# Optimization experiments

Hardware: AMD Instinct MI355X
Metric: run time of the kernel (lower is better)

Reference implementation:

```python
import jax, jax.numpy as jnp
import numpy as np

D_MODEL = 1024
N_HEADS = 16
D_HEAD = 64


def setup_inputs() -> dict:
    key = jax.random.key(0)
    ks = jax.random.split(key, 5)
    B, T = 2, 2048
    scale = 1.0 / np.sqrt(D_MODEL)
    x = jax.random.normal(ks[0], (B, T, D_MODEL), dtype=jnp.float32)
    Wq = jax.random.normal(ks[1], (N_HEADS * D_HEAD, D_MODEL), dtype=jnp.float32) * scale
    Wk = jax.random.normal(ks[2], (N_HEADS * D_HEAD, D_MODEL), dtype=jnp.float32) * scale
    Wv = jax.random.normal(ks[3], (N_HEADS * D_HEAD, D_MODEL), dtype=jnp.float32) * scale
    Wo = jax.random.normal(ks[4], (D_MODEL, N_HEADS * D_HEAD), dtype=jnp.float32) * scale
    return {"x": x, "Wq": Wq, "Wk": Wk, "Wv": Wv, "Wo": Wo}


def reference(x, Wq, Wk, Wv, Wo):
    B, T, D = x.shape
    # Linear(y = x @ W.T), then split heads: [B, H, T, d]
    def split_heads(y):
        return y.reshape(B, T, N_HEADS, D_HEAD).transpose(0, 2, 1, 3)
    q = split_heads(x @ Wq.T)
    k = split_heads(x @ Wk.T)
    v = split_heads(x @ Wv.T)
    scale = D_HEAD ** -0.5
    # Materialized [B, H, T, T] scores, as in the original module
    scores = jnp.einsum('bhtd,bhTd->bhtT', q, k) * scale
    attn = jax.nn.softmax(scores, axis=-1)
    y = jnp.einsum('bhtT,bhTd->bhtd', attn, v)
    y = y.transpose(0, 2, 1, 3).reshape(B, T, N_HEADS * D_HEAD)
    return y @ Wo.T
```

## Files before the change

### kernel.cpp

```cpp
#include <hip/hip_runtime.h>
#include <hip/hip_bf16.h>

typedef __attribute__((ext_vector_type(8))) short bf16x8;
typedef __attribute__((ext_vector_type(4))) float f32x4;
typedef unsigned short u16t;

#define DEVINL static __device__ __forceinline__

DEVINL u16t f2bf(float f) {
  union { __hip_bfloat16 h; u16t u; } cv;
  cv.h = __float2bfloat16(f);
  return cv.u;
}

DEVINL unsigned cvt_pk_bf16(float a, float b) {
  unsigned r;
  asm("v_cvt_pk_bf16_f32 %0, %1, %2" : "=v"(r) : "v"(a), "v"(b));
  return r;
}

DEVINL void async16(void* lds, const void* g) {
  __builtin_amdgcn_global_load_lds((const __attribute__((address_space(1))) void*)g,
                                   (__attribute__((address_space(3))) void*)lds,
                                   16, 0, 0);
}

__global__ __launch_bounds__(256) void convert_bf16(
    const float* __restrict__ x,  const float* __restrict__ wq,
    const float* __restrict__ wk, const float* __restrict__ wv,
    const float* __restrict__ wo,
    u16t* __restrict__ xb, u16t* __restrict__ wqb, u16t* __restrict__ wkb,
    u16t* __restrict__ wvb, u16t* __restrict__ wob) {
  const int blk = blockIdx.x;
  const float* src; u16t* dst; size_t off;
  if (blk < 4096)      { src = x;  dst = xb;  off = (size_t)blk * 1024; }
  else if (blk < 5120) { src = wq; dst = wqb; off = (size_t)(blk - 4096) * 1024; }
  else if (blk < 6144) { src = wk; dst = wkb; off = (size_t)(blk - 5120) * 1024; }
  else if (blk < 7168) { src = wv; dst = wvb; off = (size_t)(blk - 6144) * 1024; }
  else                 { src = wo; dst = wob; off = (size_t)(blk - 7168) * 1024; }
  const size_t i = off + (size_t)threadIdx.x * 4;
  const float4 v = *(const float4*)&src[i];
  ushort4 r;
  r.x = f2bf(v.x); r.y = f2bf(v.y); r.z = f2bf(v.z); r.w = f2bf(v.w);
  *(ushort4*)&dst[i] = r;
}

template <int MODE>
__global__ __launch_bounds__(256) void gemm_bt(
    const u16t* __restrict__ A, const u16t* __restrict__ B,
    void* __restrict__ C0, void* __restrict__ C1, void* __restrict__ C2,
    int M, int N, int K) {
  __shared__ u16t As[2][128 * 32];
  __shared__ u16t Bs[2][128 * 32];

  const int tid = threadIdx.x;
  const int lane = tid & 63;
  const int w = tid >> 6;
  const int wm = w >> 1, wn = w & 1;
  const int quad = lane >> 4, cl = lane & 15;
  const int m0 = blockIdx.y * 128;
  const int n0 = blockIdx.x * 128;

  const int srow = lane >> 2;
  const int scol = (lane & 3) * 8;

  f32x4 acc[4][4] = {};

  for (int k0 = 0; k0 < K; k0 += 64) {
    __syncthreads();
    #pragma unroll
    for (int p = 0; p < 2; ++p)
      #pragma unroll
      for (int ii = 0; ii < 2; ++ii) {
        const int c = w + ii * 4;
        async16(&As[p][c * 512], &A[(size_t)(m0 + c * 16 + srow) * K + k0 + p * 32 + scol]);
        async16(&Bs[p][c * 512], &B[(size_t)(n0 + c * 16 + srow) * K + k0 + p * 32 + scol]);
      }
    __syncthreads();
    #pragma unroll
    for (int p = 0; p < 2; ++p) {
      bf16x8 af[4], bfr[4];
      #pragma unroll
      for (int i = 0; i < 4; ++i)
        af[i] = *(const bf16x8*)&As[p][(wm * 64 + i * 16 + cl) * 32 + quad * 8];
      #pragma unroll
      for (int j = 0; j < 4; ++j)
        bfr[j] = *(const bf16x8*)&Bs[p][(wn * 64 + j * 16 + cl) * 32 + quad * 8];
      #pragma unroll
      for (int i = 0; i < 4; ++i)
        #pragma unroll
        for (int j = 0; j < 4; ++j)
          acc[i][j] = __builtin_amdgcn_mfma_f32_16x16x32_bf16(af[i], bfr[j], acc[i][j], 0, 0, 0);
    }
  }

  const int nz = n0 >> 10;
  #pragma unroll
  for (int i = 0; i < 4; ++i)
    #pragma unroll
    for (int j = 0; j < 4; ++j) {
      const int mb = m0 + wm * 64 + i * 16 + quad * 4;
      const int n  = n0 + wn * 64 + j * 16 + cl;
      if (MODE == 0) {
        #pragma unroll
        for (int r = 0; r < 4; ++r)
          ((float*)C0)[(size_t)(mb + r) * N + n] = acc[i][j][r];
      } else {
        const int nw = n & 1023, h = nw >> 6, d = nw & 63;
        const int b = mb >> 11, tb = mb & 2047;
        const size_t bh = (size_t)(b * 16 + h);
        if (nz == 2) {
          ushort4 v4;
          v4.x = f2bf(acc[i][j][0]); v4.y = f2bf(acc[i][j][1]);
          v4.z = f2bf(acc[i][j][2]); v4.w = f2bf(acc[i][j][3]);
          const size_t addr = (bh << 17) +
              (size_t)(((d >> 4) * 256 + (tb >> 3)) * 128 + (d & 15) * 8 + (tb & 7));
          *(ushort4*)&((u16t*)C2)[addr] = v4;
        } else if (nz == 1) {
          const size_t basea = (bh << 17) +
              (size_t)(((tb >> 4) * 8 + (d >> 3)) * 128 + (d & 7));
          #pragma unroll
          for (int r = 0; r < 4; ++r)
            ((u16t*)C1)[basea + ((tb & 15) + r) * 8] = f2bf(acc[i][j][r]);
        } else {
          #pragma unroll
          for (int r = 0; r < 4; ++r)
            ((u16t*)C0)[(bh * 2048 + tb + r) * 64 + d] =
                f2bf(acc[i][j][r] * 0.18033688011112043f);
        }
      }
    }
}

__global__ __launch_bounds__(256, 2) void flash_attn(
    const u16t* __restrict__ Q, const u16t* __restrict__ Kt,
    const u16t* __restrict__ Vt, u16t* __restrict__ Y) {
  __shared__ u16t Ps[4][32 * 136];
  const int tid = threadIdx.x;
  const int lane = tid & 63;
  const int w = tid >> 6;
  const int quad = lane >> 4, cl = lane & 15;
  const int bh = blockIdx.x;
  const int q0 = blockIdx.y * 128 + w * 32;
  const u16t* Kb = Kt + ((size_t)bh << 17);
  const u16t* Vb = Vt + ((size_t)bh << 17);

  bf16x8 aq[2][2];
  #pragma unroll
  for (int h = 0; h < 2; ++h)
    #pragma unroll
    for (int ks = 0; ks < 2; ++ks)
      aq[h][ks] = *(const bf16x8*)&Q[((size_t)bh * 2048 + q0 + 16 * h + cl) * 64 + ks * 32 + quad * 8];

  bf16x8 ones8;
  #pragma unroll
  for (int i = 0; i < 8; ++i) ones8[i] = (short)0x3F80;

  f32x4 o[2][4] = {};
  f32x4 psum[2] = {};

  u16t* Pw = &Ps[w][0];

  bf16x8 kA[2][8], kB[2][8];
  #pragma unroll
  for (int ks = 0; ks < 2; ++ks)
    #pragma unroll
    for (int js = 0; js < 8; ++js)
      kA[ks][js] = *(const bf16x8*)&Kb[(size_t)((js * 8 + ks * 4) * 128) + lane * 8];

  #define TILE_STEP(jt, kc, kn)                                               \
  {                                                                           \
              \
    f32x4 s0[8] = {}, s1[8] = {};                                             \
    __builtin_amdgcn_s_setprio(1);                                            \
    _Pragma("unroll")                                                         \
    for (int ks = 0; ks < 2; ++ks) {                                          \
      _Pragma("unroll")                                                       \
      for (int js = 0; js < 8; ++js)                                          \
        s0[js] = __builtin_amdgcn_mfma_f32_16x16x32_bf16(kc[ks][js], aq[0][ks], s0[js], 0, 0, 0); \
      _Pragma("unroll")                                                       \
      for (int js = 0; js < 8; ++js)                                          \
        s1[js] = __builtin_amdgcn_mfma_f32_16x16x32_bf16(kc[ks][js], aq[1][ks], s1[js], 0, 0, 0); \
    }                                                                         \
    __builtin_amdgcn_s_setprio(0);                                            \
       \
    _Pragma("unroll")                                                         \
    for (int js = 0; js < 8; ++js) {                                          \
      uint2 pk0, pk1;                                                         \
      pk0.x = cvt_pk_bf16(__builtin_exp2f(s0[js][0]), __builtin_exp2f(s0[js][1])); \
      pk0.y = cvt_pk_bf16(__builtin_exp2f(s0[js][2]), __builtin_exp2f(s0[js][3])); \
      *(uint2*)&Pw[cl * 136 + js * 16 + quad * 4] = pk0;                      \
      pk1.x = cvt_pk_bf16(__builtin_exp2f(s1[js][0]), __builtin_exp2f(s1[js][1])); \
      pk1.y = cvt_pk_bf16(__builtin_exp2f(s1[js][2]), __builtin_exp2f(s1[js][3])); \
      *(uint2*)&Pw[(16 + cl) * 136 + js * 16 + quad * 4] = pk1;               \
    }                                                                         \
                                 \
    bf16x8 vf[4][4];                                                          \
    _Pragma("unroll")                                                         \
    for (int ks = 0; ks < 4; ++ks)                                            \
      _Pragma("unroll")                                                       \
      for (int ds = 0; ds < 4; ++ds)                                          \
        vf[ks][ds] = *(const bf16x8*)&Vb[(size_t)((ds * 256 + (jt) * 16 + ks * 4) * 128) + lane * 8]; \
                 \
    if ((jt) + 1 < 16) {                                                      \
      _Pragma("unroll")                                                       \
      for (int ks = 0; ks < 2; ++ks)                                          \
        _Pragma("unroll")                                                     \
        for (int js = 0; js < 8; ++js)                                        \
          kn[ks][js] = *(const bf16x8*)&Kb[(size_t)((((jt) + 1) * 64 + js * 8 + ks * 4) * 128) + lane * 8]; \
    }                                                                         \
                 \
    __builtin_amdgcn_s_setprio(1);                                            \
    _Pragma("unroll")                                                         \
    for (int ks = 0; ks < 4; ++ks) {                                          \
      const bf16x8 ap0 = *(const bf16x8*)&Pw[cl * 136 + ks * 32 + quad * 8];  \
      const bf16x8 ap1 = *(const bf16x8*)&Pw[(16 + cl) * 136 + ks * 32 + quad * 8]; \
      psum[0] = __builtin_amdgcn_mfma_f32_16x16x32_bf16(ap0, ones8, psum[0], 0, 0, 0); \
      psum[1] = __builtin_amdgcn_mfma_f32_16x16x32_bf16(ap1, ones8, psum[1], 0, 0, 0); \
      _Pragma("unroll")                                                       \
      for (int ds = 0; ds < 4; ++ds) {                                        \
        o[0][ds] = __builtin_amdgcn_mfma_f32_16x16x32_bf16(ap0, vf[ks][ds], o[0][ds], 0, 0, 0); \
        o[1][ds] = __builtin_amdgcn_mfma_f32_16x16x32_bf16(ap1, vf[ks][ds], o[1][ds], 0, 0, 0); \
      }                                                                       \
    }                                                                         \
    __builtin_amdgcn_s_setprio(0);                                            \
  }

  for (int jt = 0; jt < 16; jt += 2) {
    TILE_STEP(jt, kA, kB);
    TILE_STEP(jt + 1, kB, kA);
  }
  #undef TILE_STEP

  const int b = bh >> 4, hd = bh & 15;
  #pragma unroll
  for (int h = 0; h < 2; ++h) {
    float inv[4];
    #pragma unroll
    for (int r = 0; r < 4; ++r) inv[r] = __builtin_amdgcn_rcpf(psum[h][r]);
    #pragma unroll
    for (int ds = 0; ds < 4; ++ds)
      #pragma unroll
      for (int r = 0; r < 4; ++r) {
        const int t = q0 + 16 * h + quad * 4 + r;
        const int d = ds * 16 + cl;
        Y[((size_t)b * 2048 + t) * 1024 + hd * 64 + d] = f2bf(o[h][ds][r] * inv[r]);
      }
  }
}

extern "C" void kernel_launch(void* const* d_in, const int* in_sizes, int n_in,
                              void* d_out, int out_size, void* d_ws, size_t ws_size,
                              hipStream_t stream) {
  (void)in_sizes; (void)n_in; (void)out_size; (void)ws_size;
  const float* x  = (const float*)d_in[0];
  const float* Wq = (const float*)d_in[1];
  const float* Wk = (const float*)d_in[2];
  const float* Wv = (const float*)d_in[3];
  const float* Wo = (const float*)d_in[4];

  char* ws = (char*)d_ws;
  const size_t MB = 1024 * 1024;
  u16t* xb  = (u16t*)(ws);
  u16t* Wqb = (u16t*)(ws + 8 * MB);
  u16t* Wkb = (u16t*)(ws + 10 * MB);
  u16t* Wvb = (u16t*)(ws + 12 * MB);
  u16t* Wob = (u16t*)(ws + 14 * MB);
  u16t* Qw  = (u16t*)(ws + 16 * MB);
  u16t* Ktw = (u16t*)(ws + 24 * MB);
  u16t* Vtw = (u16t*)(ws + 32 * MB);
  u16t* Yw  = xb;

  convert_bf16<<<8192, 256, 0, stream>>>(x, Wq, Wk, Wv, Wo, xb, Wqb, Wkb, Wvb, Wob);
  gemm_bt<1><<<dim3(24, 32), 256, 0, stream>>>(
      xb, Wqb, Qw, Ktw, Vtw, 4096, 3072, 1024);
  flash_attn<<<dim3(32, 16), 256, 0, stream>>>(Qw, Ktw, Vtw, Yw);
  gemm_bt<0><<<dim3(8, 32), 256, 0, stream>>>(
      Yw, Wob, d_out, d_out, d_out, 4096, 1024, 1024);
}
```

Baseline: 204.9 us.

## Double-buffer GEMM K loop, shrink out-proj tile, reorder flash-attn V loads

```diff
diff --git a/kernel.cpp b/kernel.cpp
--- a/kernel.cpp
+++ b/kernel.cpp
@@ -45,12 +45,13 @@
   *(ushort4*)&dst[i] = r;
 }
 
-template <int MODE>
+template <int MODE, int BM>
 __global__ __launch_bounds__(256) void gemm_bt(
     const u16t* __restrict__ A, const u16t* __restrict__ B,
     void* __restrict__ C0, void* __restrict__ C1, void* __restrict__ C2,
     int M, int N, int K) {
-  __shared__ u16t As[2][128 * 32];
+  constexpr int MI = BM / 32;
+  __shared__ u16t As[2][BM * 32];
   __shared__ u16t Bs[2][128 * 32];
 
   const int tid = threadIdx.x;
@@ -58,48 +59,66 @@
   const int w = tid >> 6;
   const int wm = w >> 1, wn = w & 1;
   const int quad = lane >> 4, cl = lane & 15;
-  const int m0 = blockIdx.y * 128;
+  const int m0 = blockIdx.y * BM;
   const int n0 = blockIdx.x * 128;
 
   const int srow = lane >> 2;
   const int scol = (lane & 3) * 8;
 
-  f32x4 acc[4][4] = {};
-
-  for (int k0 = 0; k0 < K; k0 += 64) {
+  f32x4 acc[MI][4] = {};
+
+  #define STAGEP(b, kp)                                                       \
+    {                                                                         \
+      _Pragma("unroll")                                                       \
+      for (int ii = 0; ii < BM / 64; ++ii) {                                  \
+        const int c = w + ii * 4;                                             \
+        async16(&As[b][c * 512],                                              \
+                &A[(size_t)(m0 + c * 16 + srow) * K + (kp) * 32 + scol]);     \
+      }                                                                       \
+      _Pragma("unroll")                                                       \
+      for (int ii = 0; ii < 2; ++ii) {                                        \
+        const int c = w + ii * 4;                                             \
+        async16(&Bs[b][c * 512],                                              \
+                &B[(size_t)(n0 + c * 16 + srow) * K + (kp) * 32 + scol]);     \
+      }                                                                       \
+    }
+
+  #define COMPUTEP(b)                                                         \
+    {                                                                         \
+      bf16x8 af[MI], bfr[4];                                                  \
+      _Pragma("unroll")                                                       \
+      for (int i = 0; i < MI; ++i)                                            \
+        af[i] = *(const bf16x8*)&As[b][(wm * (BM / 2) + i * 16 + cl) * 32 + quad * 8]; \
+      _Pragma("unroll")                                                       \
+      for (int j = 0; j < 4; ++j)                                             \
+        bfr[j] = *(const bf16x8*)&Bs[b][(wn * 64 + j * 16 + cl) * 32 + quad * 8]; \
+      _Pragma("unroll")                                                       \
+      for (int i = 0; i < MI; ++i)                                            \
+        _Pragma("unroll")                                                     \
+        for (int j = 0; j < 4; ++j)                                           \
+          acc[i][j] = __builtin_amdgcn_mfma_f32_16x16x32_bf16(af[i], bfr[j], acc[i][j], 0, 0, 0); \
+    }
+
+  const int NP = K >> 5;
+  STAGEP(0, 0);
+  __syncthreads();
+  for (int kp = 0; kp < NP; kp += 2) {
+    if (kp + 1 < NP) STAGEP(1, kp + 1);
+    COMPUTEP(0);
     __syncthreads();
-    #pragma unroll
-    for (int p = 0; p < 2; ++p)
-      #pragma unroll
-      for (int ii = 0; ii < 2; ++ii) {
-        const int c = w + ii * 4;
-        async16(&As[p][c * 512], &A[(size_t)(m0 + c * 16 + srow) * K + k0 + p * 32 + scol]);
-        async16(&Bs[p][c * 512], &B[(size_t)(n0 + c * 16 + srow) * K + k0 + p * 32 + scol]);
-      }
+    if (kp + 2 < NP) STAGEP(0, kp + 2);
+    COMPUTEP(1);
     __syncthreads();
-    #pragma unroll
-    for (int p = 0; p < 2; ++p) {
-      bf16x8 af[4], bfr[4];
-      #pragma unroll
-      for (int i = 0; i < 4; ++i)
-        af[i] = *(const bf16x8*)&As[p][(wm * 64 + i * 16 + cl) * 32 + quad * 8];
-      #pragma unroll
-      for (int j = 0; j < 4; ++j)
-        bfr[j] = *(const bf16x8*)&Bs[p][(wn * 64 + j * 16 + cl) * 32 + quad * 8];
-      #pragma unroll
-      for (int i = 0; i < 4; ++i)
-        #pragma unroll
-        for (int j = 0; j < 4; ++j)
-          acc[i][j] = __builtin_amdgcn_mfma_f32_16x16x32_bf16(af[i], bfr[j], acc[i][j], 0, 0, 0);
-    }
-  }
+  }
+  #undef STAGEP
+  #undef COMPUTEP
 
   const int nz = n0 >> 10;
   #pragma unroll
-  for (int i = 0; i < 4; ++i)
+  for (int i = 0; i < MI; ++i)
     #pragma unroll
     for (int j = 0; j < 4; ++j) {
-      const int mb = m0 + wm * 64 + i * 16 + quad * 4;
+      const int mb = m0 + wm * (BM / 2) + i * 16 + quad * 4;
       const int n  = n0 + wn * 64 + j * 16 + cl;
       if (MODE == 0) {
         #pragma unroll
@@ -135,7 +154,7 @@
 __global__ __launch_bounds__(256, 2) void flash_attn(
     const u16t* __restrict__ Q, const u16t* __restrict__ Kt,
     const u16t* __restrict__ Vt, u16t* __restrict__ Y) {
-  __shared__ u16t Ps[4][32 * 136];
+  __shared__ u16t Ps[4 * 32 * 136];
   const int tid = threadIdx.x;
   const int lane = tid & 63;
   const int w = tid >> 6;
@@ -159,7 +178,7 @@
   f32x4 o[2][4] = {};
   f32x4 psum[2] = {};
 
-  u16t* Pw = &Ps[w][0];
+  u16t* Pw = &Ps[w * 32 * 136];
 
   bf16x8 kA[2][8], kB[2][8];
   #pragma unroll
@@ -167,12 +186,12 @@
     #pragma unroll
     for (int js = 0; js < 8; ++js)
       kA[ks][js] = *(const bf16x8*)&Kb[(size_t)((js * 8 + ks * 4) * 128) + lane * 8];
+  __builtin_amdgcn_sched_barrier(0);
 
   #define TILE_STEP(jt, kc, kn)                                               \
   {                                                                           \
-              \
+                                          \
     f32x4 s0[8] = {}, s1[8] = {};                                             \
-    __builtin_amdgcn_s_setprio(1);                                            \
     _Pragma("unroll")                                                         \
     for (int ks = 0; ks < 2; ++ks) {                                          \
       _Pragma("unroll")                                                       \
@@ -182,8 +201,15 @@
       for (int js = 0; js < 8; ++js)                                          \
         s1[js] = __builtin_amdgcn_mfma_f32_16x16x32_bf16(kc[ks][js], aq[1][ks], s1[js], 0, 0, 0); \
     }                                                                         \
-    __builtin_amdgcn_s_setprio(0);                                            \
-       \
+          \
+    bf16x8 vf[4][4];                                                          \
+    _Pragma("unroll")                                                         \
+    for (int ks = 0; ks < 4; ++ks)                                            \
+      _Pragma("unroll")                                                       \
+      for (int ds = 0; ds < 4; ++ds)                                          \
+        vf[ks][ds] = *(const bf16x8*)&Vb[(size_t)((ds * 256 + (jt) * 16 + ks * 4) * 128) + lane * 8]; \
+    __builtin_amdgcn_sched_barrier(0);                                        \
+                 \
     _Pragma("unroll")                                                         \
     for (int js = 0; js < 8; ++js) {                                          \
       uint2 pk0, pk1;                                                         \
@@ -194,23 +220,17 @@
       pk1.y = cvt_pk_bf16(__builtin_exp2f(s1[js][2]), __builtin_exp2f(s1[js][3])); \
       *(uint2*)&Pw[(16 + cl) * 136 + js * 16 + quad * 4] = pk1;               \
     }                                                                         \
-                                 \
-    bf16x8 vf[4][4];                                                          \
-    _Pragma("unroll")                                                         \
-    for (int ks = 0; ks < 4; ++ks)                                            \
-      _Pragma("unroll")                                                       \
-      for (int ds = 0; ds < 4; ++ds)                                          \
-        vf[ks][ds] = *(const bf16x8*)&Vb[(size_t)((ds * 256 + (jt) * 16 + ks * 4) * 128) + lane * 8]; \
-                 \
+    __builtin_amdgcn_sched_barrier(0);                                        \
+                         \
     if ((jt) + 1 < 16) {                                                      \
       _Pragma("unroll")                                                       \
       for (int ks = 0; ks < 2; ++ks)                                          \
         _Pragma("unroll")                                                     \
         for (int js = 0; js < 8; ++js)                                        \
           kn[ks][js] = *(const bf16x8*)&Kb[(size_t)((((jt) + 1) * 64 + js * 8 + ks * 4) * 128) + lane * 8]; \
-    }                                                                         \
-                 \
-    __builtin_amdgcn_s_setprio(1);                                            \
+      __builtin_amdgcn_sched_barrier(0);                                      \
+    }                                                                         \
+      \
     _Pragma("unroll")                                                         \
     for (int ks = 0; ks < 4; ++ks) {                                          \
       const bf16x8 ap0 = *(const bf16x8*)&Pw[cl * 136 + ks * 32 + quad * 8];  \
@@ -223,7 +243,6 @@
         o[1][ds] = __builtin_amdgcn_mfma_f32_16x16x32_bf16(ap1, vf[ks][ds], o[1][ds], 0, 0, 0); \
       }                                                                       \
     }                                                                         \
-    __builtin_amdgcn_s_setprio(0);                                            \
   }
 
   for (int jt = 0; jt < 16; jt += 2) {
@@ -272,9 +291,9 @@
   u16t* Yw  = xb;
 
   convert_bf16<<<8192, 256, 0, stream>>>(x, Wq, Wk, Wv, Wo, xb, Wqb, Wkb, Wvb, Wob);
-  gemm_bt<1><<<dim3(24, 32), 256, 0, stream>>>(
+  gemm_bt<1, 128><<<dim3(24, 32), 256, 0, stream>>>(
       xb, Wqb, Qw, Ktw, Vtw, 4096, 3072, 1024);
   flash_attn<<<dim3(32, 16), 256, 0, stream>>>(Qw, Ktw, Vtw, Yw);
-  gemm_bt<0><<<dim3(8, 32), 256, 0, stream>>>(
+  gemm_bt<0, 64><<<dim3(8, 64), 256, 0, stream>>>(
       Yw, Wob, d_out, d_out, d_out, 4096, 1024, 1024);
 }
```

Result: slower. 222.7 us (+8.7%).
